# Kernel tuning notes

Measured on AMD Instinct MI355X. Metric: run time of the kernel, lower is better.

The kernel has to match this reference:

```python
import jax, jax.numpy as jnp
import numpy as np

B, T, C = 4, 2048, 1024
H = 16
DH = C // H
DFF = 4 * C


def _layernorm(x, g, b, eps=1e-5):
    mu = jnp.mean(x, axis=-1, keepdims=True)
    var = jnp.var(x, axis=-1, keepdims=True)
    return (x - mu) * jax.lax.rsqrt(var + eps) * g + b


def setup_inputs() -> dict:
    key = jax.random.key(0)
    ks = jax.random.split(key, 12)
    s = 0.02
    return {
        "x": jax.random.normal(ks[0], (B, T, C), jnp.float32),
        "Wq": jax.random.normal(ks[1], (H, C, DH), jnp.float32) * s,
        "bq": jnp.zeros((H, DH), jnp.float32),
        "Wk": jax.random.normal(ks[2], (H, C, DH), jnp.float32) * s,
        "bk": jnp.zeros((H, DH), jnp.float32),
        "Wv": jax.random.normal(ks[3], (H, C, DH), jnp.float32) * s,
        "bv": jnp.zeros((H, DH), jnp.float32),
        "Wo": jax.random.normal(ks[4], (C, C), jnp.float32) * s,
        "bo": jnp.zeros((C,), jnp.float32),
        "ln1_g": jnp.ones((C,), jnp.float32),
        "ln1_b": jnp.zeros((C,), jnp.float32),
        "ln2_g": jnp.ones((C,), jnp.float32),
        "ln2_b": jnp.zeros((C,), jnp.float32),
        "W1": jax.random.normal(ks[5], (C, DFF), jnp.float32) * s,
        "b1": jnp.zeros((DFF,), jnp.float32),
        "W2": jax.random.normal(ks[6], (DFF, C), jnp.float32) * s,
        "b2": jnp.zeros((C,), jnp.float32),
    }


def reference(x, Wq, bq, Wk, bk, Wv, bv, Wo, bo, ln1_g, ln1_b, ln2_g, ln2_b, W1, b1, W2, b2):
    # pre-norm for attention
    xn = _layernorm(x, ln1_g, ln1_b)
    # per-head projections, batched: [B,H,T,DH]
    q = jnp.einsum("btc,hcd->bhtd", xn, Wq) + bq[None, :, None, :]
    k = jnp.einsum("btc,hcd->bhtd", xn, Wk) + bk[None, :, None, :]
    v = jnp.einsum("btc,hcd->bhtd", xn, Wv) + bv[None, :, None, :]
    # FAITHFUL to source: scores / scale with scale = DH**-0.5, i.e. * sqrt(DH)
    scores = jnp.einsum("bhtd,bhsd->bhts", q, k) * jnp.sqrt(jnp.float32(DH))
    attn = jax.nn.softmax(scores, axis=-1)
    o = jnp.einsum("bhts,bhsd->bhtd", attn, v)  # [B,H,T,DH]
    # concat heads along last dim (head order matches ModuleList concat)
    o = jnp.transpose(o, (0, 2, 1, 3)).reshape(B, T, C)
    attn_out = o @ Wo + bo  # dropout is identity at eval
    x = x + attn_out
    xn2 = _layernorm(x, ln2_g, ln2_b)
    ffn = jax.nn.relu(xn2 @ W1 + b1) @ W2 + b2
    return x + ffn
```

## Files before the change

kernel.cpp:

```cpp
#include <hip/hip_runtime.h>
#include <hip/hip_bf16.h>
#include <stdint.h>

typedef unsigned short ushort_t;
typedef short short8 __attribute__((ext_vector_type(8)));
typedef unsigned short ushortx8 __attribute__((ext_vector_type(8)));
typedef float floatx4 __attribute__((ext_vector_type(4)));

__device__ __forceinline__ float b2f(ushort_t u) {
    return __uint_as_float(((unsigned int)u) << 16);
}
__device__ __forceinline__ ushort_t f2bf(float f) {
    unsigned int u = __float_as_uint(f);
    unsigned int r = u + 0x7FFFu + ((u >> 16) & 1u);
    return (ushort_t)(r >> 16);
}
__device__ __forceinline__ unsigned int pack2bf(float a, float b) {
    return (unsigned int)f2bf(a) | ((unsigned int)f2bf(b) << 16);
}
__device__ __forceinline__ void gll16(const void* g, void* l) {
    __builtin_amdgcn_global_load_lds((const __attribute__((address_space(1))) unsigned int*)g,
                                     (__attribute__((address_space(3))) unsigned int*)l,
                                     16, 0, 0);
}

__global__ void transpose_kernel(const float* __restrict__ in, ushort_t* __restrict__ out,
                                 int K, int N) {
    __shared__ float tile[32][33];
    in += (long)blockIdx.z * K * N;
    out += (long)blockIdx.z * K * N;
    int k0 = blockIdx.x * 32, n0 = blockIdx.y * 32;
    int x = threadIdx.x, y = threadIdx.y;
#pragma unroll
    for (int i = 0; i < 4; i++)
        tile[y + 8 * i][x] = in[(long)(k0 + y + 8 * i) * N + n0 + x];
    __syncthreads();
#pragma unroll
    for (int i = 0; i < 4; i++)
        out[(long)(n0 + y + 8 * i) * K + k0 + x] = f2bf(tile[x][y + 8 * i]);
}

__global__ void concat_bias_kernel(const float* __restrict__ bq, const float* __restrict__ bk,
                                   const float* __restrict__ bv, float* __restrict__ dst) {
    int i = blockIdx.x * 256 + threadIdx.x;
    dst[i] = i < 1024 ? bq[i] : (i < 2048 ? bk[i - 1024] : bv[i - 2048]);
}

__global__ __launch_bounds__(256) void ln_kernel(const float* __restrict__ in,
                                                 ushort_t* __restrict__ out,
                                                 const float* __restrict__ g,
                                                 const float* __restrict__ b) {
    long row = blockIdx.x;
    int tid = threadIdx.x;
    float4 v4 = *((const float4*)(in + row * 1024) + tid);
    float v[4] = {v4.x, v4.y, v4.z, v4.w};
    float s1 = v[0] + v[1] + v[2] + v[3];
    float s2 = v[0] * v[0] + v[1] * v[1] + v[2] * v[2] + v[3] * v[3];
#pragma unroll
    for (int m = 32; m >= 1; m >>= 1) {
        s1 += __shfl_xor(s1, m);
        s2 += __shfl_xor(s2, m);
    }
    __shared__ float r1[4], r2[4];
    int w = tid >> 6;
    if ((tid & 63) == 0) { r1[w] = s1; r2[w] = s2; }
    __syncthreads();
    s1 = r1[0] + r1[1] + r1[2] + r1[3];
    s2 = r2[0] + r2[1] + r2[2] + r2[3];
    float mu = s1 * (1.0f / 1024.0f);
    float var = s2 * (1.0f / 1024.0f) - mu * mu;
    float inv = rsqrtf(var + 1e-5f);
    float y[4];
#pragma unroll
    for (int i = 0; i < 4; i++)
        y[i] = (v[i] - mu) * inv * g[tid * 4 + i] + b[tid * 4 + i];
    unsigned int lo = (unsigned int)f2bf(y[0]) | ((unsigned int)f2bf(y[1]) << 16);
    unsigned int hi = (unsigned int)f2bf(y[2]) | ((unsigned int)f2bf(y[3]) << 16);
    *(uint2*)(out + row * 1024 + tid * 4) = make_uint2(lo, hi);
}

template <typename OutT, int RELU, int MODE>
__device__ __forceinline__ void gemm128(
    const ushort_t* __restrict__ A, int lda,
    const ushort_t* __restrict__ Bt, int ldb, int K,
    OutT* __restrict__ C, long cBatch, int ldc,
    const float* __restrict__ bias, const float* __restrict__ resid,
    ushort_t* As, ushort_t* Bs) {
    int m0 = blockIdx.x * 128, n0 = blockIdx.y * 128;
    int tid = threadIdx.x, lane = tid & 63, w = tid >> 6;
    int ln = lane & 15, quad = lane >> 4;
    int wr = w >> 1, wc = w & 1;
    int lr = lane >> 2, lc = (lane & 3) * 8;

    auto stage = [&](int k0, int buf) {
#pragma unroll
        for (int i = 0; i < 4; i++) {
            int id = w * 4 + i;
            int blk = id & 7;
            int row = blk * 16 + lr;
            if (id < 8)
                gll16(A + (long)(m0 + row) * lda + k0 + lc, As + buf * 4096 + blk * 512);
            else
                gll16(Bt + (long)(n0 + row) * ldb + k0 + lc, Bs + buf * 4096 + blk * 512);
        }
    };

    floatx4 acc[4][4];
#pragma unroll
    for (int a = 0; a < 4; a++)
#pragma unroll
        for (int bb = 0; bb < 4; bb++) acc[a][bb] = floatx4{0, 0, 0, 0};

    stage(0, 0);
    int cur = 0;
    for (int k0 = 0; k0 < K; k0 += 32, cur ^= 1) {
        __syncthreads();
        if (k0 + 32 < K) stage(k0 + 32, cur ^ 1);
        const ushort_t* Ab = As + cur * 4096;
        const ushort_t* Bb = Bs + cur * 4096;
        short8 af[4], bf[4];
#pragma unroll
        for (int j = 0; j < 4; j++) {
            af[j] = *(const short8*)(Ab + (wr * 64 + j * 16 + ln) * 32 + quad * 8);
            bf[j] = *(const short8*)(Bb + (wc * 64 + j * 16 + ln) * 32 + quad * 8);
        }
#pragma unroll
        for (int a = 0; a < 4; a++)
#pragma unroll
            for (int bb = 0; bb < 4; bb++)
                acc[a][bb] = __builtin_amdgcn_mfma_f32_16x16x32_bf16(af[a], bf[bb], acc[a][bb], 0, 0, 0);
    }
#pragma unroll
    for (int bb = 0; bb < 4; bb++) {
        int gn = n0 + wc * 64 + bb * 16 + ln;
        float bv = bias ? bias[gn] : 0.0f;
#pragma unroll
        for (int a = 0; a < 4; a++) {
#pragma unroll
            for (int r = 0; r < 4; r++) {
                int gm = m0 + wr * 64 + a * 16 + quad * 4 + r;
                float val = acc[a][bb][r] + bv;
                if (RELU) val = fmaxf(val, 0.0f);
                if constexpr (MODE == 2) {
                    int gnl = gn & 1023;
                    long off;
                    if (gn < 2048)
                        off = (long)(gn >> 10) * 8388608 + (long)(gm >> 11) * 2097152 +
                              (long)(gm & 2047) * 1024 + gnl;
                    else
                        off = 16777216L +
                              ((((long)(gm >> 11)) * 16 + (gnl >> 6)) * 64 + (gnl & 63)) * 2048 +
                              (gm & 2047);
                    C[off] = (OutT)f2bf(val);
                } else {
                    long off = (long)(gm >> 11) * cBatch + (long)(gm & 2047) * ldc + gn;
                    if (resid) val += resid[off];
                    if constexpr (sizeof(OutT) == 2)
                        C[off] = (OutT)f2bf(val);
                    else
                        C[off] = (OutT)val;
                }
            }
        }
    }
}

__global__ __launch_bounds__(256) void gemm128_qkv_kernel(
    const ushort_t* __restrict__ A, const ushort_t* __restrict__ Bt,
    ushort_t* __restrict__ C, const float* __restrict__ bias) {
    __shared__ ushort_t As[2 * 128 * 32];
    __shared__ ushort_t Bs[2 * 128 * 32];
    gemm128<ushort_t, 0, 2>(A, 1024, Bt, 1024, 1024, C, 0, 0, bias, nullptr, As, Bs);
}

__global__ __launch_bounds__(256) void gemm128_bf16_relu_kernel(
    const ushort_t* __restrict__ A, int lda, const ushort_t* __restrict__ Bt, int ldb, int K,
    ushort_t* __restrict__ C, long cBatch, int ldc, const float* __restrict__ bias) {
    __shared__ ushort_t As[2 * 128 * 32];
    __shared__ ushort_t Bs[2 * 128 * 32];
    gemm128<ushort_t, 1, 0>(A, lda, Bt, ldb, K, C, cBatch, ldc, bias, nullptr, As, Bs);
}

__global__ __launch_bounds__(256) void gemm128_f32_kernel(
    const ushort_t* __restrict__ A, int lda, const ushort_t* __restrict__ Bt, int ldb, int K,
    float* __restrict__ C, long cBatch, int ldc,
    const float* __restrict__ bias, const float* __restrict__ resid) {
    __shared__ ushort_t As[2 * 128 * 32];
    __shared__ ushort_t Bs[2 * 128 * 32];
    gemm128<float, 0, 0>(A, lda, Bt, ldb, K, C, cBatch, ldc, bias, resid, As, Bs);
}

#define PSTR 72
__global__ __launch_bounds__(512, 4) void attn_kernel(
    const ushort_t* __restrict__ q, const ushort_t* __restrict__ k,
    const ushort_t* __restrict__ vt, ushort_t* __restrict__ o) {
    __shared__ ushort_t Klds[2 * 4096];
    __shared__ ushort_t Vlds[2 * 4096];
    __shared__ ushort_t Plds[8 * 32 * PSTR];
    int flat = blockIdx.x;
    int bh = (flat & 7) * 8 + (flat >> 6);
    int xt = (flat >> 3) & 7;
    int b = bh >> 4, h = bh & 15;
    int t0 = xt * 256;
    int tid = threadIdx.x, lane = tid & 63, w = tid >> 6;
    int ln = lane & 15, quad = lane >> 4;
    int lr = lane >> 2, lc = (lane & 3) * 8;
    int bsrc = (lane & 48) + ((lane >> 4) << 2);

    const ushort_t* qbase = q + ((long)b * 2048 + t0 + w * 32) * 1024 + h * 64;
    short8 qf[2][2];
#pragma unroll
    for (int sub = 0; sub < 2; sub++)
#pragma unroll
        for (int s = 0; s < 2; s++) {
            ushortx8 t = *(const ushortx8*)(qbase + (long)(sub * 16 + ln) * 1024 + s * 32 + quad * 8);
#pragma unroll
            for (int j = 0; j < 8; j++) qf[sub][s][j] = (short)f2bf(b2f(t[j]) * 8.0f);
        }

    floatx4 O[2][4];
    float m_i[2] = {-1e30f, -1e30f}, l_i[2] = {0.0f, 0.0f};
#pragma unroll
    for (int sub = 0; sub < 2; sub++)
#pragma unroll
        for (int i = 0; i < 4; i++) O[sub][i] = floatx4{0, 0, 0, 0};

    ushort_t* Pw = Plds + w * 32 * PSTR;
    long krow0 = (long)b * 2048 * 1024 + h * 64;
    const ushort_t* vbase = vt + (long)bh * 64 * 2048;

    auto stage = [&](int kv0, int buf) {
#pragma unroll
        for (int i = 0; i < 2; i++) {
            int id = w * 2 + i;
            int s = (id >> 2) & 1, qt = id & 3;
            int row = qt * 16 + lr;
            if (id < 8)
                gll16(k + krow0 + (long)(kv0 + row) * 1024 + s * 32 + lc,
                      Klds + buf * 4096 + s * 2048 + qt * 512);
            else
                gll16(vbase + (long)row * 2048 + kv0 + s * 32 + lc,
                      Vlds + buf * 4096 + s * 2048 + qt * 512);
        }
    };

    stage(0, 0);
    int cur = 0;
    for (int t32 = 0; t32 < 32; t32++, cur ^= 1) {
        __syncthreads();
        if (t32 < 31) stage((t32 + 1) * 64, cur ^ 1);
        const ushort_t* Kb = Klds + cur * 4096;
        const ushort_t* Vb = Vlds + cur * 4096;

        float alpha[2];
#pragma unroll
        for (int sub = 0; sub < 2; sub++) {
            floatx4 Z[4];
#pragma unroll
            for (int nc = 0; nc < 4; nc++) Z[nc] = floatx4{0, 0, 0, 0};
#pragma unroll
            for (int s = 0; s < 2; s++)
#pragma unroll
                for (int nc = 0; nc < 4; nc++) {
                    short8 kf = *(const short8*)(Kb + s * 2048 + (nc * 16 + ln) * 32 + quad * 8);
                    Z[nc] = __builtin_amdgcn_mfma_f32_16x16x32_bf16(kf, qf[sub][s], Z[nc], 0, 0, 0);
                }
            float mx = -1e30f;
#pragma unroll
            for (int nc = 0; nc < 4; nc++)
#pragma unroll
                for (int r = 0; r < 4; r++) mx = fmaxf(mx, Z[nc][r]);
            mx = fmaxf(mx, __shfl_xor(mx, 16));
            mx = fmaxf(mx, __shfl_xor(mx, 32));
            float nm = fmaxf(m_i[sub], mx);
            alpha[sub] = __expf(m_i[sub] - nm);
            m_i[sub] = nm;
            float rs = 0.0f;
            ushort_t* Ps = Pw + sub * 16 * PSTR + ln * PSTR;
#pragma unroll
            for (int nc = 0; nc < 4; nc++) {
                float p0 = __expf(Z[nc][0] - nm), p1 = __expf(Z[nc][1] - nm);
                float p2 = __expf(Z[nc][2] - nm), p3 = __expf(Z[nc][3] - nm);
                rs += (p0 + p1) + (p2 + p3);
                *(uint2*)(Ps + nc * 16 + quad * 4) = make_uint2(pack2bf(p0, p1), pack2bf(p2, p3));
            }
            rs += __shfl_xor(rs, 16);
            rs += __shfl_xor(rs, 32);
            l_i[sub] = l_i[sub] * alpha[sub] + rs;
        }
#pragma unroll
        for (int sub = 0; sub < 2; sub++) {
#pragma unroll
            for (int r = 0; r < 4; r++) {
                float ar = __shfl(alpha[sub], bsrc + r);
#pragma unroll
                for (int dc = 0; dc < 4; dc++) O[sub][dc][r] *= ar;
            }
            short8 pf[2];
#pragma unroll
            for (int s = 0; s < 2; s++)
                pf[s] = *(const short8*)(Pw + (sub * 16 + ln) * PSTR + s * 32 + quad * 8);
#pragma unroll
            for (int s = 0; s < 2; s++)
#pragma unroll
                for (int dc = 0; dc < 4; dc++) {
                    short8 vf = *(const short8*)(Vb + s * 2048 + (dc * 16 + ln) * 32 + quad * 8);
                    O[sub][dc] = __builtin_amdgcn_mfma_f32_16x16x32_bf16(pf[s], vf, O[sub][dc], 0, 0, 0);
                }
        }
    }
#pragma unroll
    for (int sub = 0; sub < 2; sub++)
#pragma unroll
        for (int r = 0; r < 4; r++) {
            float inv = 1.0f / __shfl(l_i[sub], bsrc + r);
            int t = t0 + w * 32 + sub * 16 + quad * 4 + r;
            ushort_t* orow = o + ((long)b * 2048 + t) * 1024 + h * 64;
#pragma unroll
            for (int dc = 0; dc < 4; dc++) orow[dc * 16 + ln] = f2bf(O[sub][dc][r] * inv);
        }
}

extern "C" void kernel_launch(void* const* d_in, const int* in_sizes, int n_in,
                              void* d_out, int out_size, void* d_ws, size_t ws_size,
                              hipStream_t stream) {
    const float* x   = (const float*)d_in[0];
    const float* Wq  = (const float*)d_in[1];
    const float* bq  = (const float*)d_in[2];
    const float* Wk  = (const float*)d_in[3];
    const float* bk  = (const float*)d_in[4];
    const float* Wv  = (const float*)d_in[5];
    const float* bv  = (const float*)d_in[6];
    const float* Wo  = (const float*)d_in[7];
    const float* bo  = (const float*)d_in[8];
    const float* g1  = (const float*)d_in[9];
    const float* be1 = (const float*)d_in[10];
    const float* g2  = (const float*)d_in[11];
    const float* be2 = (const float*)d_in[12];
    const float* W1  = (const float*)d_in[13];
    const float* b1  = (const float*)d_in[14];
    const float* W2  = (const float*)d_in[15];
    const float* b2  = (const float*)d_in[16];
    float* out = (float*)d_out;

    const long MB = 1 << 20;
    char* w = (char*)d_ws;
    ushort_t* xn  = (ushort_t*)(w);
    float*    x2  = (float*)(w + 16 * MB);
    ushort_t* qb  = (ushort_t*)(w + 48 * MB);
    ushort_t* kb  = (ushort_t*)(w + 64 * MB);
    ushort_t* vtb = (ushort_t*)(w + 80 * MB);
    ushort_t* xn2 = qb;
    ushort_t* h1  = (ushort_t*)(w + 64 * MB);
    ushort_t* WqT = (ushort_t*)(w + 96 * MB);
    ushort_t* WkT = (ushort_t*)(w + 98 * MB);
    ushort_t* WvT = (ushort_t*)(w + 100 * MB);
    ushort_t* WoT = (ushort_t*)(w + 102 * MB);
    ushort_t* W1T = (ushort_t*)(w + 104 * MB);
    ushort_t* W2T = (ushort_t*)(w + 112 * MB);
    float* biasCat = x2;

    dim3 tb(32, 8);
    transpose_kernel<<<dim3(32, 2, 16), tb, 0, stream>>>(Wq, WqT, 1024, 64);
    transpose_kernel<<<dim3(32, 2, 16), tb, 0, stream>>>(Wk, WkT, 1024, 64);
    transpose_kernel<<<dim3(32, 2, 16), tb, 0, stream>>>(Wv, WvT, 1024, 64);
    transpose_kernel<<<dim3(32, 32, 1), tb, 0, stream>>>(Wo, WoT, 1024, 1024);
    transpose_kernel<<<dim3(32, 128, 1), tb, 0, stream>>>(W1, W1T, 1024, 4096);
    transpose_kernel<<<dim3(128, 32, 1), tb, 0, stream>>>(W2, W2T, 4096, 1024);
    concat_bias_kernel<<<12, 256, 0, stream>>>(bq, bk, bv, biasCat);

    ln_kernel<<<8192, 256, 0, stream>>>(x, xn, g1, be1);
    gemm128_qkv_kernel<<<dim3(64, 24), 256, 0, stream>>>(xn, WqT, qb, biasCat);
    attn_kernel<<<512, 512, 0, stream>>>(qb, kb, vtb, xn );
    gemm128_f32_kernel<<<dim3(64, 8), 256, 0, stream>>>(xn, 1024, WoT, 1024, 1024,
                                                        x2, 2048L * 1024, 1024, bo, x);
    ln_kernel<<<8192, 256, 0, stream>>>((const float*)x2, xn2, g2, be2);
    gemm128_bf16_relu_kernel<<<dim3(64, 16), 256, 0, stream>>>(
        xn2, 1024, W1T, 1024, 1024, h1, 2048L * 2048, 2048, b1);
    gemm128_f32_kernel<<<dim3(64, 8), 256, 0, stream>>>(
        h1, 2048, W2T, 4096, 2048, out, 2048L * 1024, 1024, b2, x2);
    gemm128_bf16_relu_kernel<<<dim3(64, 16), 256, 0, stream>>>(
        xn2, 1024, W1T + 2048L * 1024, 1024, 1024, h1, 2048L * 2048, 2048, b1 + 2048);
    gemm128_f32_kernel<<<dim3(64, 8), 256, 0, stream>>>(
        h1, 2048, W2T + 2048, 4096, 2048, out, 2048L * 1024, 1024, nullptr, out);
}
```

Measured before the change: 632.5 us.

## Swizzle attention LDS layouts and share K/V fragments across both sub-tiles

```diff
diff --git a/kernel.cpp b/kernel.cpp
--- a/kernel.cpp
+++ b/kernel.cpp
@@ -190,13 +190,12 @@
     gemm128<float, 0, 0>(A, lda, Bt, ldb, K, C, cBatch, ldc, bias, resid, As, Bs);
 }
 
-#define PSTR 72
 __global__ __launch_bounds__(512, 4) void attn_kernel(
     const ushort_t* __restrict__ q, const ushort_t* __restrict__ k,
     const ushort_t* __restrict__ vt, ushort_t* __restrict__ o) {
     __shared__ ushort_t Klds[2 * 4096];
     __shared__ ushort_t Vlds[2 * 4096];
-    __shared__ ushort_t Plds[8 * 32 * PSTR];
+    __shared__ ushort_t Plds[8 * 32 * 64];
     int flat = blockIdx.x;
     int bh = (flat & 7) * 8 + (flat >> 6);
     int xt = (flat >> 3) & 7;
@@ -204,8 +203,11 @@
     int t0 = xt * 256;
     int tid = threadIdx.x, lane = tid & 63, w = tid >> 6;
     int ln = lane & 15, quad = lane >> 4;
-    int lr = lane >> 2, lc = (lane & 3) * 8;
+    int lr = lane >> 2, lq = lane & 3;
     int bsrc = (lane & 48) + ((lane >> 4) << 2);
+    int rsw = (ln >> 1) & 3;
+    int ssw = (lr >> 1) & 3;
+    int p7 = ln & 7;
 
     const ushort_t* qbase = q + ((long)b * 2048 + t0 + w * 32) * 1024 + h * 64;
     short8 qf[2][2];
@@ -225,7 +227,7 @@
 #pragma unroll
         for (int i = 0; i < 4; i++) O[sub][i] = floatx4{0, 0, 0, 0};
 
-    ushort_t* Pw = Plds + w * 32 * PSTR;
+    ushort_t* Pw = Plds + w * 32 * 64;
     long krow0 = (long)b * 2048 * 1024 + h * 64;
     const ushort_t* vbase = vt + (long)bh * 64 * 2048;
 
@@ -235,11 +237,12 @@
             int id = w * 2 + i;
             int s = (id >> 2) & 1, qt = id & 3;
             int row = qt * 16 + lr;
+            int cs = ((lq ^ ssw) << 3);
             if (id < 8)
-                gll16(k + krow0 + (long)(kv0 + row) * 1024 + s * 32 + lc,
+                gll16(k + krow0 + (long)(kv0 + row) * 1024 + s * 32 + cs,
                       Klds + buf * 4096 + s * 2048 + qt * 512);
             else
-                gll16(vbase + (long)row * 2048 + kv0 + s * 32 + lc,
+                gll16(vbase + (long)row * 2048 + kv0 + s * 32 + cs,
                       Vlds + buf * 4096 + s * 2048 + qt * 512);
         }
     };
@@ -252,62 +255,70 @@
         const ushort_t* Kb = Klds + cur * 4096;
         const ushort_t* Vb = Vlds + cur * 4096;
 
+        floatx4 Z[2][4];
+#pragma unroll
+        for (int sub = 0; sub < 2; sub++)
+#pragma unroll
+            for (int nc = 0; nc < 4; nc++) Z[sub][nc] = floatx4{0, 0, 0, 0};
+#pragma unroll
+        for (int s = 0; s < 2; s++)
+#pragma unroll
+            for (int nc = 0; nc < 4; nc++) {
+                short8 kf = *(const short8*)(Kb + s * 2048 + (nc * 16 + ln) * 32 + ((quad ^ rsw) << 3));
+                Z[0][nc] = __builtin_amdgcn_mfma_f32_16x16x32_bf16(kf, qf[0][s], Z[0][nc], 0, 0, 0);
+                Z[1][nc] = __builtin_amdgcn_mfma_f32_16x16x32_bf16(kf, qf[1][s], Z[1][nc], 0, 0, 0);
+            }
+
         float alpha[2];
 #pragma unroll
         for (int sub = 0; sub < 2; sub++) {
-            floatx4 Z[4];
-#pragma unroll
-            for (int nc = 0; nc < 4; nc++) Z[nc] = floatx4{0, 0, 0, 0};
-#pragma unroll
-            for (int s = 0; s < 2; s++)
-#pragma unroll
-                for (int nc = 0; nc < 4; nc++) {
-                    short8 kf = *(const short8*)(Kb + s * 2048 + (nc * 16 + ln) * 32 + quad * 8);
-                    Z[nc] = __builtin_amdgcn_mfma_f32_16x16x32_bf16(kf, qf[sub][s], Z[nc], 0, 0, 0);
-                }
             float mx = -1e30f;
 #pragma unroll
             for (int nc = 0; nc < 4; nc++)
 #pragma unroll
-                for (int r = 0; r < 4; r++) mx = fmaxf(mx, Z[nc][r]);
+                for (int r = 0; r < 4; r++) mx = fmaxf(mx, Z[sub][nc][r]);
             mx = fmaxf(mx, __shfl_xor(mx, 16));
             mx = fmaxf(mx, __shfl_xor(mx, 32));
             float nm = fmaxf(m_i[sub], mx);
             alpha[sub] = __expf(m_i[sub] - nm);
             m_i[sub] = nm;
             float rs = 0.0f;
-            ushort_t* Ps = Pw + sub * 16 * PSTR + ln * PSTR;
+            ushort_t* Ps = Pw + (sub * 16 + ln) * 64;
 #pragma unroll
             for (int nc = 0; nc < 4; nc++) {
-                float p0 = __expf(Z[nc][0] - nm), p1 = __expf(Z[nc][1] - nm);
-                float p2 = __expf(Z[nc][2] - nm), p3 = __expf(Z[nc][3] - nm);
+                float p0 = __expf(Z[sub][nc][0] - nm), p1 = __expf(Z[sub][nc][1] - nm);
+                float p2 = __expf(Z[sub][nc][2] - nm), p3 = __expf(Z[sub][nc][3] - nm);
                 rs += (p0 + p1) + (p2 + p3);
-                *(uint2*)(Ps + nc * 16 + quad * 4) = make_uint2(pack2bf(p0, p1), pack2bf(p2, p3));
+                int col = (((nc * 2 + (quad >> 1)) ^ p7) << 3) | ((quad & 1) << 2);
+                *(uint2*)(Ps + col) = make_uint2(pack2bf(p0, p1), pack2bf(p2, p3));
             }
             rs += __shfl_xor(rs, 16);
             rs += __shfl_xor(rs, 32);
             l_i[sub] = l_i[sub] * alpha[sub] + rs;
         }
 #pragma unroll
-        for (int sub = 0; sub < 2; sub++) {
+        for (int sub = 0; sub < 2; sub++)
 #pragma unroll
             for (int r = 0; r < 4; r++) {
                 float ar = __shfl(alpha[sub], bsrc + r);
 #pragma unroll
                 for (int dc = 0; dc < 4; dc++) O[sub][dc][r] *= ar;
             }
-            short8 pf[2];
+        short8 pf[2][2];
+#pragma unroll
+        for (int sub = 0; sub < 2; sub++)
 #pragma unroll
             for (int s = 0; s < 2; s++)
-                pf[s] = *(const short8*)(Pw + (sub * 16 + ln) * PSTR + s * 32 + quad * 8);
-#pragma unroll
-            for (int s = 0; s < 2; s++)
-#pragma unroll
-                for (int dc = 0; dc < 4; dc++) {
-                    short8 vf = *(const short8*)(Vb + s * 2048 + (dc * 16 + ln) * 32 + quad * 8);
-                    O[sub][dc] = __builtin_amdgcn_mfma_f32_16x16x32_bf16(pf[s], vf, O[sub][dc], 0, 0, 0);
-                }
-        }
+                pf[sub][s] = *(const short8*)(Pw + (sub * 16 + ln) * 64 +
+                                              ((((s << 2) + quad) ^ p7) << 3));
+#pragma unroll
+        for (int s = 0; s < 2; s++)
+#pragma unroll
+            for (int dc = 0; dc < 4; dc++) {
+                short8 vf = *(const short8*)(Vb + s * 2048 + (dc * 16 + ln) * 32 + ((quad ^ rsw) << 3));
+                O[0][dc] = __builtin_amdgcn_mfma_f32_16x16x32_bf16(pf[0][s], vf, O[0][dc], 0, 0, 0);
+                O[1][dc] = __builtin_amdgcn_mfma_f32_16x16x32_bf16(pf[1][s], vf, O[1][dc], 0, 0, 0);
+            }
     }
 #pragma unroll
     for (int sub = 0; sub < 2; sub++)
```

Result: faster. 599.4 us (-5.2%).
